# Optimization experiments

Hardware: AMD Instinct MI355X
Metric: run time of the kernel (lower is better)

Reference implementation:

```python
import jax, jax.numpy as jnp
import numpy as np

T, B, W, L = 256, 128, 1024, 2


def setup_inputs() -> dict:
    key = jax.random.key(0)
    k1, k2, k3, k4 = jax.random.split(key, 4)
    scale = 1.0 / np.sqrt(W)
    return {
        "xs": jax.random.normal(k1, (T, B, W), dtype=jnp.float32),
        "resets": jax.random.bernoulli(k2, 0.05, (T, B)),
        "Wx": jax.random.normal(k3, (L, W, 4 * W), dtype=jnp.float32) * scale,
        "Wh": jax.random.normal(k4, (L, W, 4 * W), dtype=jnp.float32) * scale,
        "b": jnp.zeros((L, 4 * W), dtype=jnp.float32),
    }


def reference(xs, resets, Wx, Wh, b):
    # xs: [T,B,W], resets: [T,B] bool, Wx/Wh: [L,W,4W], b: [L,4W]
    L_, B_, W_ = Wx.shape[0], xs.shape[1], xs.shape[2]

    def step(carry, inp):
        cs, hs = carry          # each [L,B,W]
        x, r = inp              # [B,W], [B]
        m = r[None, :, None]    # reset -> reinitialize state to zeros
        cs = jnp.where(m, 0.0, cs)
        hs = jnp.where(m, 0.0, hs)
        y = x
        new_cs, new_hs = [], []
        for l in range(L_):
            z = y @ Wx[l] + hs[l] @ Wh[l] + b[l]          # [B,4W]
            i, f, g, o = jnp.split(z, 4, axis=-1)
            i = jax.nn.sigmoid(i)
            f = jax.nn.sigmoid(f)
            g = jnp.tanh(g)
            o = jax.nn.sigmoid(o)
            c = f * cs[l] + i * g
            h = o * jnp.tanh(c)
            new_cs.append(c)
            new_hs.append(h)
            y = h
        return (jnp.stack(new_cs), jnp.stack(new_hs)), y

    carry0 = (jnp.zeros((L_, B_, W_), xs.dtype), jnp.zeros((L_, B_, W_), xs.dtype))
    _, ys = jax.lax.scan(step, carry0, (xs, resets))
    return ys  # [T,B,W]
```

## Files before the change

### kernel.cpp

```cpp
#include <hip/hip_runtime.h>

#define T_   256
#define B_   128
#define W_   1024
#define G_   4096
#define NWG  256
#define NTHR 512
#define SLE  131072
#define NSLOT 258
#define SSTRIDE 127

typedef __bf16 bf16x8 __attribute__((ext_vector_type(8)));
typedef __bf16 bf16x4 __attribute__((ext_vector_type(4)));
typedef float  f32x4  __attribute__((ext_vector_type(4)));
typedef unsigned int u32x2 __attribute__((ext_vector_type(2)));
typedef unsigned int u32x4 __attribute__((ext_vector_type(4)));

#define ZSTRIDE   18
#define LDS_Z0    131072
#define LDS_Z1    140288
#define LDS_BIAS  149504
#define LDS_TOTAL 149632

__device__ __forceinline__ float sigf(float x)   { return 1.f / (1.f + __expf(-x)); }
__device__ __forceinline__ float tanhf_(float x) { return 1.f - 2.f / (__expf(2.f * x) + 1.f); }

__device__ __forceinline__ int read_reset(const void* r, int mode, int idx) {
  if (mode == 0) return ((const int*)r)[idx] != 0;
  if (mode == 1) return ((const unsigned char*)r)[idx] != 0;
  return ((const float*)r)[idx] != 0.0f;
}

#define GLD_C(dst, p) asm volatile("global_load_dwordx4 %0, %1, off sc0 sc1" : "=v"(dst) : "v"(p))
#define GLD_N(dst, p) asm volatile("global_load_dwordx4 %0, %1, off"         : "=v"(dst) : "v"(p))
#define GLD_H(dst, p) do { if constexpr (MODE == 0 || MODE == 3) { GLD_N(dst, p); } else { GLD_C(dst, p); } } while (0)
#define WAITV(N) do { asm volatile("s_waitcnt vmcnt(" #N ")" ::: "memory"); \
                      __builtin_amdgcn_sched_barrier(0); } while (0)

__device__ __forceinline__ void grid_sync(unsigned* bar, unsigned target, int wg) {
  __syncthreads();
  if (threadIdx.x == 0) {
    unsigned* sub = bar + 96 + (wg & 7) * 32;
    bool resetter = false;
    unsigned a = __hip_atomic_fetch_add(sub, 1u, __ATOMIC_RELAXED, __HIP_MEMORY_SCOPE_AGENT);
    if (a == 31) {
      unsigned ra = __hip_atomic_fetch_add(bar, 1u, __ATOMIC_RELAXED, __HIP_MEMORY_SCOPE_AGENT);
      if (ra == 7) {
        #pragma unroll
        for (int i = 0; i < 8; ++i)
          __hip_atomic_store(bar + 96 + i * 32, 0u, __ATOMIC_RELAXED, __HIP_MEMORY_SCOPE_AGENT);
        __hip_atomic_store(bar, 0u, __ATOMIC_RELAXED, __HIP_MEMORY_SCOPE_AGENT);
        asm volatile("s_waitcnt vmcnt(0)" ::: "memory");
        __hip_atomic_store(bar + 32, target, __ATOMIC_RELAXED, __HIP_MEMORY_SCOPE_AGENT);
        resetter = true;
      }
    }
    if (!resetter) {
      while (__hip_atomic_load(bar + 32, __ATOMIC_RELAXED, __HIP_MEMORY_SCOPE_AGENT) < target)
        __builtin_amdgcn_s_sleep(2);
    }
  }
  __syncthreads();
}

template <int MODE>
__global__ __launch_bounds__(NTHR, 2)
void lstm_scan(const float* __restrict__ xs, const void* __restrict__ rst,
               const float* __restrict__ Wx, const float* __restrict__ Wh,
               const float* __restrict__ bb, float* __restrict__ out,
               unsigned short* xsb_u, unsigned short* r0_u, unsigned short* r1_u,
               unsigned* bar) {
  extern __shared__ char smem[];
  __bf16* xsb = (__bf16*)xsb_u;
  __bf16* ring0 = (__bf16*)r0_u;
  __bf16* ring1 = (__bf16*)r1_u;
  const int tid = threadIdx.x;
  const int wg  = blockIdx.x;
  const int u0  = wg * 4;

  if (wg == 0) {
    const int* ri = (const int*)rst;
    unsigned f = 0;
    for (int i = tid; i < (T_ * B_) / 4; i += NTHR) {
      unsigned v = (unsigned)ri[i];
      if (v > 1u) f |= 1u;
      if (v != 0u && v != 0x3F800000u) f |= 2u;
    }
    if (f) atomicOr(bar + 64, f);
  }
  if (MODE == 0 || MODE == 1) {
    const int gt = wg * NTHR + tid;
    const f32x4* src = (const f32x4*)xs;
    for (int i = gt; i < (T_ * B_ * W_) / 4; i += NWG * NTHR) {
      f32x4 v = src[i];
      bf16x4 o;
      o[0] = (__bf16)v[0]; o[1] = (__bf16)v[1]; o[2] = (__bf16)v[2]; o[3] = (__bf16)v[3];
      u32x2 ov = __builtin_bit_cast(u32x2, o);
      asm volatile("global_store_dwordx2 %0, %1, off sc0 sc1" :: "v"((bf16x4*)xsb + i), "v"(ov) : "memory");
    }
  }
  {
    const int gt = wg * NTHR + tid;
    const u32x4 z4 = {0u, 0u, 0u, 0u};
    if constexpr (MODE == 0 || MODE == 3) {
      for (int i = gt; i < SLE / 8; i += NWG * NTHR) {
        asm volatile("global_store_dwordx4 %0, %1, off sc0 sc1" :: "v"((u32x4*)r0_u + i), "v"(z4) : "memory");
        asm volatile("global_store_dwordx4 %0, %1, off sc0 sc1" :: "v"((u32x4*)r1_u + i), "v"(z4) : "memory");
      }
    } else {
      for (int i = gt; i < 65536; i += NWG * NTHR)
        asm volatile("global_store_dwordx4 %0, %1, off sc0 sc1" :: "v"((u32x4*)r0_u + i), "v"(z4) : "memory");
    }
  }
  {
    const int c  = tid & 15, kc = tid >> 4;
    const int col0 = ((c >> 2) << 10) + u0 + (c & 3);
    const int sw = (c & 7) << 4;
    const float* srcs[4] = { Wx, Wh, Wx + (size_t)W_ * G_, Wh + (size_t)W_ * G_ };
    for (int m = 0; m < 4; ++m) {
      const float* s = srcs[m] + col0;
      char* base = smem + m * 32768 + c * 2048;
      for (int kk = 0; kk < 32; ++kk) {
        const int k = kc * 32 + kk;
        *(__bf16*)(base + ((k * 2) ^ sw)) = (__bf16)s[(size_t)k * G_];
      }
    }
    if (tid < 32) {
      const int cc = tid & 15, l = tid >> 4;
      const int col = ((cc >> 2) << 10) + u0 + (cc & 3);
      ((float*)(smem + LDS_BIAS))[l * 16 + cc] = bb[l * G_ + col];
    }
  }
  asm volatile("s_waitcnt vmcnt(0)" ::: "memory");
  grid_sync(bar, 1u, wg);
  const unsigned mf = __hip_atomic_load(bar + 64, __ATOMIC_RELAXED, __HIP_MEMORY_SCOPE_AGENT);
  const int rmode = ((mf & 1u) == 0) ? 0 : (((mf & 2u) == 0) ? 2 : 1);

  const int lane = tid & 63, wv = tid >> 6;
  const int rq   = wv & 3;
  const int kh   = wv >> 2;
  const int lrow = lane & 15;
  const int kgrp = lane >> 4;
  const int c16  = lane & 15;
  const int swz  = (c16 & 7) << 4;
  const char* wlds = smem + c16 * 2048;
  const int row0 = (rq << 5) + lrow;
  const int row1 = row0 + 16;
  const int gb = tid >> 2, du = tid & 3;
  const int ofs = (kh << 9) + (kgrp << 3);

  float c0 = 0.f, c1 = 0.f;
  int slot_r = 0, slot_w = SSTRIDE;

  for (int p = 0; p <= T_; ++p) {
    if constexpr (MODE == 1 || MODE == 2) { slot_r = (p + 1) & 1; slot_w = p & 1; }
    const __bf16* h0r = ring0 + (size_t)slot_r * SLE;
    __bf16*       h0w = ring0 + (size_t)slot_w * SLE;
    const __bf16* h1r = ring1 + (size_t)slot_r * SLE;
    __bf16*       h1w = ring1 + (size_t)slot_w * SLE;
    const int tx = (p < T_) ? p : (T_ - 1);
    int r0a = (p < T_) ? read_reset(rst, rmode, p * B_ + row0) : 0;
    int r0b = (p < T_) ? read_reset(rst, rmode, p * B_ + row1) : 0;
    int r1a = (p >= 1) ? read_reset(rst, rmode, (p - 1) * B_ + row0) : 0;
    int r1b = (p >= 1) ? read_reset(rst, rmode, (p - 1) * B_ + row1) : 0;

    const __bf16* pX0  = xsb + (size_t)tx * (B_ * W_) + row0 * W_ + ofs;
    const __bf16* pX1  = xsb + (size_t)tx * (B_ * W_) + row1 * W_ + ofs;
    const float*  pXf0 = xs  + (size_t)tx * (B_ * W_) + row0 * W_ + ofs;
    const float*  pXf1 = xs  + (size_t)tx * (B_ * W_) + row1 * W_ + ofs;
    const __bf16* pH00 = h0r + row0 * W_ + ofs;
    const __bf16* pH01 = h0r + row1 * W_ + ofs;
    const __bf16* pH10 = h1r + row0 * W_ + ofs;
    const __bf16* pH11 = h1r + row1 * W_ + ofs;

    f32x4 a00 = {0.f,0.f,0.f,0.f}, a01 = {0.f,0.f,0.f,0.f};
    f32x4 a10 = {0.f,0.f,0.f,0.f}, a11 = {0.f,0.f,0.f,0.f};
    const bf16x8 z8 = {};

    asm volatile("" :: "v"(r0a), "v"(r0b), "v"(r1a), "v"(r1b));
    asm volatile("s_waitcnt vmcnt(0)" ::: "memory");

    if constexpr (MODE == 0 || MODE == 1) {
      f32x4 Px0,Px1,P00,P01,P10,P11, Qx0,Qx1,Q00,Q01,Q10,Q11;
      GLD_N(Px0, pX0);  GLD_N(Px1, pX1);
      GLD_H(P00, pH00); GLD_H(P01, pH01); GLD_H(P10, pH10); GLD_H(P11, pH11);

#define KSTEP_B(CX0,CX1,C00,C01,C10,C11, NX0,NX1,N00,N01,N10,N11, KI, ISNEXT) \
      { \
        if (ISNEXT) { \
          const int no = ((KI) + 1) * 32; \
          GLD_N(NX0, pX0 + no);  GLD_N(NX1, pX1 + no); \
          GLD_H(N00, pH00 + no); GLD_H(N01, pH01 + no); \
          GLD_H(N10, pH10 + no); GLD_H(N11, pH11 + no); \
        } \
        const int koff = ((kh << 10) + ((KI) << 6) + (kgrp << 4)) ^ swz; \
        bf16x8 w0 = *(const bf16x8*)(wlds +     0 + koff); \
        bf16x8 w1 = *(const bf16x8*)(wlds + 32768 + koff); \
        bf16x8 w2 = *(const bf16x8*)(wlds + 65536 + koff); \
        bf16x8 w3 = *(const bf16x8*)(wlds + 98304 + koff); \
        if (ISNEXT) { WAITV(6); } else { WAITV(0); } \
        bf16x8 ax0 = __builtin_bit_cast(bf16x8, CX0); \
        bf16x8 ax1 = __builtin_bit_cast(bf16x8, CX1); \
        bf16x8 b00 = __builtin_bit_cast(bf16x8, C00); \
        bf16x8 b01 = __builtin_bit_cast(bf16x8, C01); \
        bf16x8 b10 = __builtin_bit_cast(bf16x8, C10); \
        bf16x8 b11 = __builtin_bit_cast(bf16x8, C11); \
        a00 = __builtin_amdgcn_mfma_f32_16x16x32_bf16(ax0, w0, a00, 0, 0, 0); \
        a00 = __builtin_amdgcn_mfma_f32_16x16x32_bf16(r0a ? z8 : b00, w1, a00, 0, 0, 0); \
        a10 = __builtin_amdgcn_mfma_f32_16x16x32_bf16(b00, w2, a10, 0, 0, 0); \
        a10 = __builtin_amdgcn_mfma_f32_16x16x32_bf16(r1a ? z8 : b10, w3, a10, 0, 0, 0); \
        a01 = __builtin_amdgcn_mfma_f32_16x16x32_bf16(ax1, w0, a01, 0, 0, 0); \
        a01 = __builtin_amdgcn_mfma_f32_16x16x32_bf16(r0b ? z8 : b01, w1, a01, 0, 0, 0); \
        a11 = __builtin_amdgcn_mfma_f32_16x16x32_bf16(b01, w2, a11, 0, 0, 0); \
        a11 = __builtin_amdgcn_mfma_f32_16x16x32_bf16(r1b ? z8 : b11, w3, a11, 0, 0, 0); \
      }

      #pragma unroll
      for (int kp = 0; kp < 8; ++kp) {
        KSTEP_B(Px0,Px1,P00,P01,P10,P11, Qx0,Qx1,Q00,Q01,Q10,Q11, 2*kp,   1);
        KSTEP_B(Qx0,Qx1,Q00,Q01,Q10,Q11, Px0,Px1,P00,P01,P10,P11, 2*kp+1, (kp < 7));
      }
#undef KSTEP_B
    } else {
      f32x4 Pxa0,Pxb0,Pxa1,Pxb1,P00,P01,P10,P11, Qxa0,Qxb0,Qxa1,Qxb1,Q00,Q01,Q10,Q11;
      GLD_N(Pxa0, pXf0); GLD_N(Pxb0, pXf0 + 4);
      GLD_N(Pxa1, pXf1); GLD_N(Pxb1, pXf1 + 4);
      GLD_H(P00, pH00);  GLD_H(P01, pH01); GLD_H(P10, pH10); GLD_H(P11, pH11);

#define KSTEP_F(CXA0,CXB0,CXA1,CXB1,C00,C01,C10,C11, NXA0,NXB0,NXA1,NXB1,N00,N01,N10,N11, KI, ISNEXT) \
      { \
        if (ISNEXT) { \
          const int no = ((KI) + 1) * 32; \
          GLD_N(NXA0, pXf0 + no); GLD_N(NXB0, pXf0 + no + 4); \
          GLD_N(NXA1, pXf1 + no); GLD_N(NXB1, pXf1 + no + 4); \
          GLD_H(N00, pH00 + no);  GLD_H(N01, pH01 + no); \
          GLD_H(N10, pH10 + no);  GLD_H(N11, pH11 + no); \
        } \
        const int koff = ((kh << 10) + ((KI) << 6) + (kgrp << 4)) ^ swz; \
        bf16x8 w0 = *(const bf16x8*)(wlds +     0 + koff); \
        bf16x8 w1 = *(const bf16x8*)(wlds + 32768 + koff); \
        bf16x8 w2 = *(const bf16x8*)(wlds + 65536 + koff); \
        bf16x8 w3 = *(const bf16x8*)(wlds + 98304 + koff); \
        if (ISNEXT) { WAITV(8); } else { WAITV(0); } \
        bf16x8 ax0, ax1; \
        _Pragma("unroll") \
        for (int j = 0; j < 4; ++j) { \
          ax0[j] = (__bf16)CXA0[j]; ax0[4+j] = (__bf16)CXB0[j]; \
          ax1[j] = (__bf16)CXA1[j]; ax1[4+j] = (__bf16)CXB1[j]; \
        } \
        bf16x8 b00 = __builtin_bit_cast(bf16x8, C00); \
        bf16x8 b01 = __builtin_bit_cast(bf16x8, C01); \
        bf16x8 b10 = __builtin_bit_cast(bf16x8, C10); \
        bf16x8 b11 = __builtin_bit_cast(bf16x8, C11); \
        a00 = __builtin_amdgcn_mfma_f32_16x16x32_bf16(ax0, w0, a00, 0, 0, 0); \
        a00 = __builtin_amdgcn_mfma_f32_16x16x32_bf16(r0a ? z8 : b00, w1, a00, 0, 0, 0); \
        a10 = __builtin_amdgcn_mfma_f32_16x16x32_bf16(b00, w2, a10, 0, 0, 0); \
        a10 = __builtin_amdgcn_mfma_f32_16x16x32_bf16(r1a ? z8 : b10, w3, a10, 0, 0, 0); \
        a01 = __builtin_amdgcn_mfma_f32_16x16x32_bf16(ax1, w0, a01, 0, 0, 0); \
        a01 = __builtin_amdgcn_mfma_f32_16x16x32_bf16(r0b ? z8 : b01, w1, a01, 0, 0, 0); \
        a11 = __builtin_amdgcn_mfma_f32_16x16x32_bf16(b01, w2, a11, 0, 0, 0); \
        a11 = __builtin_amdgcn_mfma_f32_16x16x32_bf16(r1b ? z8 : b11, w3, a11, 0, 0, 0); \
      }

      #pragma unroll
      for (int kp = 0; kp < 8; ++kp) {
        KSTEP_F(Pxa0,Pxb0,Pxa1,Pxb1,P00,P01,P10,P11, Qxa0,Qxb0,Qxa1,Qxb1,Q00,Q01,Q10,Q11, 2*kp,   1);
        KSTEP_F(Qxa0,Qxb0,Qxa1,Qxb1,Q00,Q01,Q10,Q11, Pxa0,Pxb0,Pxa1,Pxb1,P00,P01,P10,P11, 2*kp+1, (kp < 7));
      }
#undef KSTEP_F
    }

    {
      float* z0 = (float*)(smem + LDS_Z0);
      float* z1 = (float*)(smem + LDS_Z1);
      const int zr0 = (rq << 5) + (kgrp << 2);
      const int zr1 = zr0 + 16;
      if (kh == 0) {
        if (p < T_) {
          #pragma unroll
          for (int v = 0; v < 4; ++v) { z0[(zr0+v)*ZSTRIDE + c16] = a00[v]; z0[(zr1+v)*ZSTRIDE + c16] = a01[v]; }
        }
        if (p >= 1) {
          #pragma unroll
          for (int v = 0; v < 4; ++v) { z1[(zr0+v)*ZSTRIDE + c16] = a10[v]; z1[(zr1+v)*ZSTRIDE + c16] = a11[v]; }
        }
      }
      __syncthreads();
      if (kh == 1) {
        if (p < T_) {
          #pragma unroll
          for (int v = 0; v < 4; ++v) { z0[(zr0+v)*ZSTRIDE + c16] += a00[v]; z0[(zr1+v)*ZSTRIDE + c16] += a01[v]; }
        }
        if (p >= 1) {
          #pragma unroll
          for (int v = 0; v < 4; ++v) { z1[(zr0+v)*ZSTRIDE + c16] += a10[v]; z1[(zr1+v)*ZSTRIDE + c16] += a11[v]; }
        }
      }
      __syncthreads();
    }

    const float* bz = (const float*)(smem + LDS_BIAS);
    if (p < T_) {
      const float* z0 = (const float*)(smem + LDS_Z0);
      const float zi = z0[gb * ZSTRIDE + du]      + bz[du];
      const float zf = z0[gb * ZSTRIDE + 4 + du]  + bz[4 + du];
      const float zg = z0[gb * ZSTRIDE + 8 + du]  + bz[8 + du];
      const float zo = z0[gb * ZSTRIDE + 12 + du] + bz[12 + du];
      const float ii = sigf(zi), ff = sigf(zf), gg = tanhf_(zg), oo = sigf(zo);
      if (read_reset(rst, rmode, p * B_ + gb)) c0 = 0.f;
      c0 = ff * c0 + ii * gg;
      const float h = oo * tanhf_(c0);
      unsigned hv = (unsigned)__builtin_bit_cast(unsigned short, (__bf16)h);
      asm volatile("global_store_short %0, %1, off sc0 sc1" :: "v"(h0w + gb * W_ + u0 + du), "v"(hv) : "memory");
    }
    if (p >= 1) {
      const float* z1 = (const float*)(smem + LDS_Z1);
      const float zi = z1[gb * ZSTRIDE + du]      + bz[16 + du];
      const float zf = z1[gb * ZSTRIDE + 4 + du]  + bz[20 + du];
      const float zg = z1[gb * ZSTRIDE + 8 + du]  + bz[24 + du];
      const float zo = z1[gb * ZSTRIDE + 12 + du] + bz[28 + du];
      const float ii = sigf(zi), ff = sigf(zf), gg = tanhf_(zg), oo = sigf(zo);
      if (read_reset(rst, rmode, (p - 1) * B_ + gb)) c1 = 0.f;
      c1 = ff * c1 + ii * gg;
      const float h = oo * tanhf_(c1);
      unsigned hv = (unsigned)__builtin_bit_cast(unsigned short, (__bf16)h);
      asm volatile("global_store_short %0, %1, off sc0 sc1" :: "v"(h1w + gb * W_ + u0 + du), "v"(hv) : "memory");
      out[(size_t)(p - 1) * (B_ * W_) + gb * W_ + u0 + du] = h;
    }
    if constexpr (MODE == 0 || MODE == 3) {
      slot_r = slot_w;
      slot_w += SSTRIDE; if (slot_w >= NSLOT) slot_w -= NSLOT;
    }
    asm volatile("s_waitcnt vmcnt(0)" ::: "memory");
    grid_sync(bar, (unsigned)(p + 2), wg);
  }
}

extern "C" void kernel_launch(void* const* d_in, const int* in_sizes, int n_in,
                              void* d_out, int out_size, void* d_ws, size_t ws_size,
                              hipStream_t stream) {
  const float* xs  = (const float*)d_in[0];
  const void*  rst = (const void*)d_in[1];
  const float* Wx  = (const float*)d_in[2];
  const float* Wh  = (const float*)d_in[3];
  const float* bb  = (const float*)d_in[4];
  float* out = (float*)d_out;

  char* ws = (char*)d_ws;
  const size_t slb       = (size_t)SLE * 2;
  const size_t xsb_bytes = (size_t)T_ * B_ * W_ * 2;
  const size_t ring_bytes = 2 * (size_t)NSLOT * slb;
  const size_t need0 = 4096 + xsb_bytes + ring_bytes;
  const size_t need3 = 4096 + ring_bytes;
  const size_t need1 = 4096 + xsb_bytes + 4 * slb;

  unsigned* bar = (unsigned*)ws;
  (void)hipMemsetAsync(bar, 0, 4096, stream);

  unsigned short *xsb, *r0, *r1;
  int mode;
  if (ws_size >= need0) {
    mode = 0;
    xsb = (unsigned short*)(ws + 4096);
    r0  = (unsigned short*)(ws + 4096 + xsb_bytes);
    r1  = r0 + (size_t)NSLOT * SLE;
  } else if (ws_size >= need3) {
    mode = 3;
    xsb = (unsigned short*)(ws + 4096);
    r0  = (unsigned short*)(ws + 4096);
    r1  = r0 + (size_t)NSLOT * SLE;
  } else if (ws_size >= need1) {
    mode = 1;
    xsb = (unsigned short*)(ws + 4096);
    r0  = (unsigned short*)(ws + 4096 + xsb_bytes);
    r1  = r0 + 2 * SLE;
  } else {
    mode = 2;
    xsb = (unsigned short*)(ws + 4096);
    r0  = (unsigned short*)(ws + 4096);
    r1  = r0 + 2 * SLE;
  }

  void* args[] = { (void*)&xs, (void*)&rst, (void*)&Wx, (void*)&Wh, (void*)&bb, (void*)&out,
                   (void*)&xsb, (void*)&r0, (void*)&r1, (void*)&bar };

  if (mode == 0) {
    (void)hipFuncSetAttribute(reinterpret_cast<const void*>(&lstm_scan<0>),
                              hipFuncAttributeMaxDynamicSharedMemorySize, LDS_TOTAL);
    (void)hipLaunchCooperativeKernel(reinterpret_cast<const void*>(&lstm_scan<0>),
                                     dim3(NWG), dim3(NTHR), args, LDS_TOTAL, stream);
  } else if (mode == 3) {
    (void)hipFuncSetAttribute(reinterpret_cast<const void*>(&lstm_scan<3>),
                              hipFuncAttributeMaxDynamicSharedMemorySize, LDS_TOTAL);
    (void)hipLaunchCooperativeKernel(reinterpret_cast<const void*>(&lstm_scan<3>),
                                     dim3(NWG), dim3(NTHR), args, LDS_TOTAL, stream);
  } else if (mode == 1) {
    (void)hipFuncSetAttribute(reinterpret_cast<const void*>(&lstm_scan<1>),
                              hipFuncAttributeMaxDynamicSharedMemorySize, LDS_TOTAL);
    (void)hipLaunchCooperativeKernel(reinterpret_cast<const void*>(&lstm_scan<1>),
                                     dim3(NWG), dim3(NTHR), args, LDS_TOTAL, stream);
  } else {
    (void)hipFuncSetAttribute(reinterpret_cast<const void*>(&lstm_scan<2>),
                              hipFuncAttributeMaxDynamicSharedMemorySize, LDS_TOTAL);
    (void)hipLaunchCooperativeKernel(reinterpret_cast<const void*>(&lstm_scan<2>),
                                     dim3(NWG), dim3(NTHR), args, LDS_TOTAL, stream);
  }
}
```

Before: 7.208 ms.

## Add workspace mode reading layer-1 hidden state from fp32 output

Adds a new fallback mode that drops the bf16 ring for the layer-1 hidden state and instead reads the previous h1 directly from the fp32 output buffer written two steps earlier, converting it to bf16 on the fly. This lets a medium-sized workspace use a many-slot ring for layer 0 instead of the double-buffered mode 1. Output stores use cache-bypassing stores so other workgroups see them after the grid barrier. It adds extra fp32 loads and conversions per k-step in exchange for less workspace.

Measured after the change: 7.224 ms. Within noise of the previous version (+0.2%).

```diff
diff --git a/kernel.cpp b/kernel.cpp
--- a/kernel.cpp
+++ b/kernel.cpp
@@ -74,9 +74,11 @@
   __bf16* xsb = (__bf16*)xsb_u;
   __bf16* ring0 = (__bf16*)r0_u;
   __bf16* ring1 = (__bf16*)r1_u;
+  const float* h1zf = (const float*)r1_u;
   const int tid = threadIdx.x;
   const int wg  = blockIdx.x;
   const int u0  = wg * 4;
+  constexpr int NS = (MODE == 4) ? 257 : NSLOT;
 
   if (wg == 0) {
     const int* ri = (const int*)rst;
@@ -88,7 +90,7 @@
     }
     if (f) atomicOr(bar + 64, f);
   }
-  if (MODE == 0 || MODE == 1) {
+  if constexpr (MODE == 0) {
     const int gt = wg * NTHR + tid;
     const f32x4* src = (const f32x4*)xs;
     for (int i = gt; i < (T_ * B_ * W_) / 4; i += NWG * NTHR) {
@@ -107,6 +109,11 @@
         asm volatile("global_store_dwordx4 %0, %1, off sc0 sc1" :: "v"((u32x4*)r0_u + i), "v"(z4) : "memory");
         asm volatile("global_store_dwordx4 %0, %1, off sc0 sc1" :: "v"((u32x4*)r1_u + i), "v"(z4) : "memory");
       }
+    } else if constexpr (MODE == 4) {
+      for (int i = gt; i < SLE / 8; i += NWG * NTHR)
+        asm volatile("global_store_dwordx4 %0, %1, off sc0 sc1" :: "v"((u32x4*)r0_u + i), "v"(z4) : "memory");
+      for (int i = gt; i < SLE / 4; i += NWG * NTHR)
+        asm volatile("global_store_dwordx4 %0, %1, off sc0 sc1" :: "v"((u32x4*)r1_u + i), "v"(z4) : "memory");
     } else {
       for (int i = gt; i < 65536; i += NWG * NTHR)
         asm volatile("global_store_dwordx4 %0, %1, off sc0 sc1" :: "v"((u32x4*)r0_u + i), "v"(z4) : "memory");
@@ -153,7 +160,7 @@
   int slot_r = 0, slot_w = SSTRIDE;
 
   for (int p = 0; p <= T_; ++p) {
-    if constexpr (MODE == 1 || MODE == 2) { slot_r = (p + 1) & 1; slot_w = p & 1; }
+    if constexpr (MODE == 2) { slot_r = (p + 1) & 1; slot_w = p & 1; }
     const __bf16* h0r = ring0 + (size_t)slot_r * SLE;
     __bf16*       h0w = ring0 + (size_t)slot_w * SLE;
     const __bf16* h1r = ring1 + (size_t)slot_r * SLE;
@@ -180,7 +187,7 @@
     asm volatile("" :: "v"(r0a), "v"(r0b), "v"(r1a), "v"(r1b));
     asm volatile("s_waitcnt vmcnt(0)" ::: "memory");
 
-    if constexpr (MODE == 0 || MODE == 1) {
+    if constexpr (MODE == 0) {
       f32x4 Px0,Px1,P00,P01,P10,P11, Qx0,Qx1,Q00,Q01,Q10,Q11;
       GLD_N(Px0, pX0);  GLD_N(Px1, pX1);
       GLD_H(P00, pH00); GLD_H(P01, pH01); GLD_H(P10, pH10); GLD_H(P11, pH11);
@@ -221,7 +228,7 @@
         KSTEP_B(Qx0,Qx1,Q00,Q01,Q10,Q11, Px0,Px1,P00,P01,P10,P11, 2*kp+1, (kp < 7));
       }
 #undef KSTEP_B
-    } else {
+    } else if constexpr (MODE == 2 || MODE == 3) {
       f32x4 Pxa0,Pxb0,Pxa1,Pxb1,P00,P01,P10,P11, Qxa0,Qxb0,Qxa1,Qxb1,Q00,Q01,Q10,Q11;
       GLD_N(Pxa0, pXf0); GLD_N(Pxb0, pXf0 + 4);
       GLD_N(Pxa1, pXf1); GLD_N(Pxb1, pXf1 + 4);
@@ -245,8 +252,8 @@
         bf16x8 ax0, ax1; \
         _Pragma("unroll") \
         for (int j = 0; j < 4; ++j) { \
-          ax0[j] = (__bf16)CXA0[j]; ax0[4+j] = (__bf16)CXB0[j]; \
-          ax1[j] = (__bf16)CXA1[j]; ax1[4+j] = (__bf16)CXB1[j]; \
+          ax0[j]=(__bf16)CXA0[j]; ax0[4+j]=(__bf16)CXB0[j]; \
+          ax1[j]=(__bf16)CXA1[j]; ax1[4+j]=(__bf16)CXB1[j]; \
         } \
         bf16x8 b00 = __builtin_bit_cast(bf16x8, C00); \
         bf16x8 b01 = __builtin_bit_cast(bf16x8, C01); \
@@ -268,6 +275,60 @@
         KSTEP_F(Qxa0,Qxb0,Qxa1,Qxb1,Q00,Q01,Q10,Q11, Pxa0,Pxb0,Pxa1,Pxb1,P00,P01,P10,P11, 2*kp+1, (kp < 7));
       }
 #undef KSTEP_F
+    } else {
+      const float* h1f = (p >= 2) ? (out + (size_t)(p - 2) * (B_ * W_)) : h1zf;
+      const float* pH10f = h1f + row0 * W_ + ofs;
+      const float* pH11f = h1f + row1 * W_ + ofs;
+      f32x4 Pxa0,Pxb0,Pxa1,Pxb1,P00,P01,Pha,Phb,Phc,Phd;
+      f32x4 Qxa0,Qxb0,Qxa1,Qxb1,Q00,Q01,Qha,Qhb,Qhc,Qhd;
+      GLD_N(Pxa0, pXf0);  GLD_N(Pxb0, pXf0 + 4);
+      GLD_N(Pxa1, pXf1);  GLD_N(Pxb1, pXf1 + 4);
+      GLD_N(P00, pH00);   GLD_N(P01, pH01);
+      GLD_N(Pha, pH10f);  GLD_N(Phb, pH10f + 4);
+      GLD_N(Phc, pH11f);  GLD_N(Phd, pH11f + 4);
+
+#define KSTEP_M4(CXA0,CXB0,CXA1,CXB1,C00,C01,CHA,CHB,CHC,CHD, NXA0,NXB0,NXA1,NXB1,N00,N01,NHA,NHB,NHC,NHD, KI, ISNEXT) \
+      { \
+        if (ISNEXT) { \
+          const int no = ((KI) + 1) * 32; \
+          GLD_N(NXA0, pXf0 + no);  GLD_N(NXB0, pXf0 + no + 4); \
+          GLD_N(NXA1, pXf1 + no);  GLD_N(NXB1, pXf1 + no + 4); \
+          GLD_N(N00, pH00 + no);   GLD_N(N01, pH01 + no); \
+          GLD_N(NHA, pH10f + no);  GLD_N(NHB, pH10f + no + 4); \
+          GLD_N(NHC, pH11f + no);  GLD_N(NHD, pH11f + no + 4); \
+        } \
+        const int koff = ((kh << 10) + ((KI) << 6) + (kgrp << 4)) ^ swz; \
+        bf16x8 w0 = *(const bf16x8*)(wlds +     0 + koff); \
+        bf16x8 w1 = *(const bf16x8*)(wlds + 32768 + koff); \
+        bf16x8 w2 = *(const bf16x8*)(wlds + 65536 + koff); \
+        bf16x8 w3 = *(const bf16x8*)(wlds + 98304 + koff); \
+        if (ISNEXT) { WAITV(10); } else { WAITV(0); } \
+        bf16x8 ax0, ax1, bh0, bh1; \
+        _Pragma("unroll") \
+        for (int j = 0; j < 4; ++j) { \
+          ax0[j]=(__bf16)CXA0[j]; ax0[4+j]=(__bf16)CXB0[j]; \
+          ax1[j]=(__bf16)CXA1[j]; ax1[4+j]=(__bf16)CXB1[j]; \
+          bh0[j]=(__bf16)CHA[j];  bh0[4+j]=(__bf16)CHB[j]; \
+          bh1[j]=(__bf16)CHC[j];  bh1[4+j]=(__bf16)CHD[j]; \
+        } \
+        bf16x8 b00 = __builtin_bit_cast(bf16x8, C00); \
+        bf16x8 b01 = __builtin_bit_cast(bf16x8, C01); \
+        a00 = __builtin_amdgcn_mfma_f32_16x16x32_bf16(ax0, w0, a00, 0, 0, 0); \
+        a00 = __builtin_amdgcn_mfma_f32_16x16x32_bf16(r0a ? z8 : b00, w1, a00, 0, 0, 0); \
+        a10 = __builtin_amdgcn_mfma_f32_16x16x32_bf16(b00, w2, a10, 0, 0, 0); \
+        a10 = __builtin_amdgcn_mfma_f32_16x16x32_bf16(r1a ? z8 : bh0, w3, a10, 0, 0, 0); \
+        a01 = __builtin_amdgcn_mfma_f32_16x16x32_bf16(ax1, w0, a01, 0, 0, 0); \
+        a01 = __builtin_amdgcn_mfma_f32_16x16x32_bf16(r0b ? z8 : b01, w1, a01, 0, 0, 0); \
+        a11 = __builtin_amdgcn_mfma_f32_16x16x32_bf16(b01, w2, a11, 0, 0, 0); \
+        a11 = __builtin_amdgcn_mfma_f32_16x16x32_bf16(r1b ? z8 : bh1, w3, a11, 0, 0, 0); \
+      }
+
+      #pragma unroll
+      for (int kp = 0; kp < 8; ++kp) {
+        KSTEP_M4(Pxa0,Pxb0,Pxa1,Pxb1,P00,P01,Pha,Phb,Phc,Phd, Qxa0,Qxb0,Qxa1,Qxb1,Q00,Q01,Qha,Qhb,Qhc,Qhd, 2*kp,   1);
+        KSTEP_M4(Qxa0,Qxb0,Qxa1,Qxb1,Q00,Q01,Qha,Qhb,Qhc,Qhd, Pxa0,Pxb0,Pxa1,Pxb1,P00,P01,Pha,Phb,Phc,Phd, 2*kp+1, (kp < 7));
+      }
+#undef KSTEP_M4
     }
 
     {
@@ -323,13 +384,18 @@
       if (read_reset(rst, rmode, (p - 1) * B_ + gb)) c1 = 0.f;
       c1 = ff * c1 + ii * gg;
       const float h = oo * tanhf_(c1);
-      unsigned hv = (unsigned)__builtin_bit_cast(unsigned short, (__bf16)h);
-      asm volatile("global_store_short %0, %1, off sc0 sc1" :: "v"(h1w + gb * W_ + u0 + du), "v"(hv) : "memory");
-      out[(size_t)(p - 1) * (B_ * W_) + gb * W_ + u0 + du] = h;
-    }
-    if constexpr (MODE == 0 || MODE == 3) {
+      if constexpr (MODE == 4) {
+        asm volatile("global_store_dword %0, %1, off sc0 sc1"
+                     :: "v"(out + (size_t)(p - 1) * (B_ * W_) + gb * W_ + u0 + du), "v"(h) : "memory");
+      } else {
+        unsigned hv = (unsigned)__builtin_bit_cast(unsigned short, (__bf16)h);
+        asm volatile("global_store_short %0, %1, off sc0 sc1" :: "v"(h1w + gb * W_ + u0 + du), "v"(hv) : "memory");
+        out[(size_t)(p - 1) * (B_ * W_) + gb * W_ + u0 + du] = h;
+      }
+    }
+    if constexpr (MODE != 2) {
       slot_r = slot_w;
-      slot_w += SSTRIDE; if (slot_w >= NSLOT) slot_w -= NSLOT;
+      slot_w += SSTRIDE; if (slot_w >= NS) slot_w -= NS;
     }
     asm volatile("s_waitcnt vmcnt(0)" ::: "memory");
     grid_sync(bar, (unsigned)(p + 2), wg);
@@ -349,10 +415,9 @@
   char* ws = (char*)d_ws;
   const size_t slb       = (size_t)SLE * 2;
   const size_t xsb_bytes = (size_t)T_ * B_ * W_ * 2;
-  const size_t ring_bytes = 2 * (size_t)NSLOT * slb;
-  const size_t need0 = 4096 + xsb_bytes + ring_bytes;
-  const size_t need3 = 4096 + ring_bytes;
-  const size_t need1 = 4096 + xsb_bytes + 4 * slb;
+  const size_t need0 = 4096 + xsb_bytes + 2 * (size_t)NSLOT * slb;
+  const size_t need3 = 4096 + 2 * (size_t)NSLOT * slb;
+  const size_t need4 = 4096 + (size_t)SLE * 4 + 257 * slb;
 
   unsigned* bar = (unsigned*)ws;
   (void)hipMemsetAsync(bar, 0, 4096, stream);
@@ -369,11 +434,11 @@
     xsb = (unsigned short*)(ws + 4096);
     r0  = (unsigned short*)(ws + 4096);
     r1  = r0 + (size_t)NSLOT * SLE;
-  } else if (ws_size >= need1) {
-    mode = 1;
+  } else if (ws_size >= need4) {
+    mode = 4;
     xsb = (unsigned short*)(ws + 4096);
-    r0  = (unsigned short*)(ws + 4096 + xsb_bytes);
-    r1  = r0 + 2 * SLE;
+    r1  = (unsigned short*)(ws + 4096);
+    r0  = (unsigned short*)(ws + 4096 + (size_t)SLE * 4);
   } else {
     mode = 2;
     xsb = (unsigned short*)(ws + 4096);
@@ -384,25 +449,12 @@
   void* args[] = { (void*)&xs, (void*)&rst, (void*)&Wx, (void*)&Wh, (void*)&bb, (void*)&out,
                    (void*)&xsb, (void*)&r0, (void*)&r1, (void*)&bar };
 
-  if (mode == 0) {
-    (void)hipFuncSetAttribute(reinterpret_cast<const void*>(&lstm_scan<0>),
-                              hipFuncAttributeMaxDynamicSharedMemorySize, LDS_TOTAL);
-    (void)hipLaunchCooperativeKernel(reinterpret_cast<const void*>(&lstm_scan<0>),
-                                     dim3(NWG), dim3(NTHR), args, LDS_TOTAL, stream);
-  } else if (mode == 3) {
-    (void)hipFuncSetAttribute(reinterpret_cast<const void*>(&lstm_scan<3>),
-                              hipFuncAttributeMaxDynamicSharedMemorySize, LDS_TOTAL);
-    (void)hipLaunchCooperativeKernel(reinterpret_cast<const void*>(&lstm_scan<3>),
-                                     dim3(NWG), dim3(NTHR), args, LDS_TOTAL, stream);
-  } else if (mode == 1) {
-    (void)hipFuncSetAttribute(reinterpret_cast<const void*>(&lstm_scan<1>),
-                              hipFuncAttributeMaxDynamicSharedMemorySize, LDS_TOTAL);
-    (void)hipLaunchCooperativeKernel(reinterpret_cast<const void*>(&lstm_scan<1>),
-                                     dim3(NWG), dim3(NTHR), args, LDS_TOTAL, stream);
-  } else {
-    (void)hipFuncSetAttribute(reinterpret_cast<const void*>(&lstm_scan<2>),
-                              hipFuncAttributeMaxDynamicSharedMemorySize, LDS_TOTAL);
-    (void)hipLaunchCooperativeKernel(reinterpret_cast<const void*>(&lstm_scan<2>),
-                                     dim3(NWG), dim3(NTHR), args, LDS_TOTAL, stream);
-  }
+  const void* fn;
+  if      (mode == 0) fn = reinterpret_cast<const void*>(&lstm_scan<0>);
+  else if (mode == 3) fn = reinterpret_cast<const void*>(&lstm_scan<3>);
+  else if (mode == 4) fn = reinterpret_cast<const void*>(&lstm_scan<4>);
+  else                fn = reinterpret_cast<const void*>(&lstm_scan<2>);
+
+  (void)hipFuncSetAttribute(fn, hipFuncAttributeMaxDynamicSharedMemorySize, LDS_TOTAL);
+  (void)hipLaunchCooperativeKernel(fn, dim3(NWG), dim3(NTHR), args, LDS_TOTAL, stream);
 }
```
